# Kernel optimization log

Hardware: AMD Instinct MI355X
Metric: run time of the kernel (lower is better)

## Reference

```python
import jax, jax.numpy as jnp
import numpy as np

B, H, W = 64, 128, 128
K_SIS, K_RANGE = 0.5, 0.3
PSI_SCALE = 0.05
SKIP_W = 0.1
ALPHA_MAX = 0.5
SIGMA, KSIZE = 1.0, 5
DN = ('NCHW', 'OIHW', 'NCHW')


def conv2d(x, w, b, pad):
    y = jax.lax.conv_general_dilated(x, w, (1, 1), [(pad, pad), (pad, pad)], dimension_numbers=DN)
    return y + b[None, :, None, None]


def group_norm(x, groups, gamma, beta, eps=1e-5):
    Bc, C, Hc, Wc = x.shape
    xr = x.reshape(Bc, groups, C // groups, Hc, Wc)
    mu = xr.mean(axis=(2, 3, 4), keepdims=True)
    var = xr.var(axis=(2, 3, 4), keepdims=True)
    xn = ((xr - mu) / jnp.sqrt(var + eps)).reshape(Bc, C, Hc, Wc)
    return xn * gamma[None, :, None, None] + beta[None, :, None, None]


def coords():
    xs = jnp.linspace(-1.0, 1.0, W)
    ys = jnp.linspace(-1.0, 1.0, H)
    X, Y = jnp.meshgrid(xs, ys, indexing='xy')  # (H, W)
    r = jnp.sqrt(X * X + Y * Y)
    phi = jnp.arctan2(Y, X)
    polar = jnp.stack([r, jnp.cos(phi), jnp.sin(phi)], axis=0)  # (3,H,W)
    base_grid = jnp.stack([X, Y], axis=-1)  # (H,W,2)
    return polar, r, base_grid


def gaussian_blur(x):
    off = jnp.arange(KSIZE, dtype=jnp.float32) - (KSIZE - 1) / 2.0
    k1 = jnp.exp(-off * off / (2.0 * SIGMA * SIGMA))
    k1 = k1 / k1.sum()
    p = KSIZE // 2
    xp = jnp.pad(x, ((0, 0), (0, 0), (p, p), (p, p)), mode='reflect')
    xh = jax.lax.conv_general_dilated(xp, k1.reshape(1, 1, 1, KSIZE), (1, 1), [(0, 0), (0, 0)], dimension_numbers=DN)
    return jax.lax.conv_general_dilated(xh, k1.reshape(1, 1, KSIZE, 1), (1, 1), [(0, 0), (0, 0)], dimension_numbers=DN)


def grad_x(a, dx):  # along W (last axis), np.gradient style
    left = a[..., 1:2] - a[..., 0:1]
    mid = (a[..., 2:] - a[..., :-2]) * 0.5
    right = a[..., -1:] - a[..., -2:-1]
    return jnp.concatenate([left, mid, right], axis=-1) / dx


def grad_y(a, dy):  # along H
    top = a[..., 1:2, :] - a[..., 0:1, :]
    mid = (a[..., 2:, :] - a[..., :-2, :]) * 0.5
    bot = a[..., -1:, :] - a[..., -2:-1, :]
    return jnp.concatenate([top, mid, bot], axis=-2) / dy


def soft_clamp(a):
    return ALPHA_MAX * jnp.tanh(a / ALPHA_MAX)


def grid_sample_bilinear_border(img, grid):
    # img (B,1,H,W), grid (B,H,W,2) in [-1,1], align_corners=True, border pad
    Bc, _, Hc, Wc = img.shape
    px = (grid[..., 0] + 1.0) * 0.5 * (Wc - 1)
    py = (grid[..., 1] + 1.0) * 0.5 * (Hc - 1)
    x0 = jnp.floor(px)
    y0 = jnp.floor(py)
    wx = px - x0
    wy = py - y0
    x0i = jnp.clip(x0.astype(jnp.int32), 0, Wc - 1)
    x1i = jnp.clip(x0i + 1, 0, Wc - 1)
    y0i = jnp.clip(y0.astype(jnp.int32), 0, Hc - 1)
    y1i = jnp.clip(y0i + 1, 0, Hc - 1)
    im = img[:, 0]
    bidx = jnp.arange(Bc)[:, None, None]
    g = lambda yy, xx: im[bidx, yy, xx]
    out = (g(y0i, x0i) * (1 - wx) * (1 - wy) + g(y0i, x1i) * wx * (1 - wy)
           + g(y1i, x0i) * (1 - wx) * wy + g(y1i, x1i) * wx * wy)
    return out[:, None, :, :]


def _conv_init(key, shape, scale=None):
    fan_in = shape[1] * shape[2] * shape[3]
    s = scale if scale is not None else 1.0 / np.sqrt(fan_in)
    return jax.random.normal(key, shape, dtype=jnp.float32) * s


def setup_inputs() -> dict:
    key = jax.random.key(0)
    ks = jax.random.split(key, 16)
    d = {'image': jax.random.uniform(ks[0], (B, 1, H, W), dtype=jnp.float32)}
    # KPredictor params
    d['kw1'] = _conv_init(ks[1], (32, 4, 3, 3)); d['kb1'] = jnp.zeros((32,), jnp.float32)
    d['kg1'] = jnp.ones((32,), jnp.float32); d['kbeta1'] = jnp.zeros((32,), jnp.float32)
    d['kw2'] = _conv_init(ks[2], (32, 32, 3, 3)); d['kb2'] = jnp.zeros((32,), jnp.float32)
    d['kg2'] = jnp.ones((32,), jnp.float32); d['kbeta2'] = jnp.zeros((32,), jnp.float32)
    d['kw3'] = _conv_init(ks[3], (16, 32, 3, 3)); d['kb3'] = jnp.zeros((16,), jnp.float32)
    d['kg3'] = jnp.ones((16,), jnp.float32); d['kbeta3'] = jnp.zeros((16,), jnp.float32)
    d['kw4'] = _conv_init(ks[4], (1, 16, 1, 1), scale=0.02); d['kb4'] = jnp.zeros((1,), jnp.float32)
    # PsiResidualPredictor params
    d['pw1'] = _conv_init(ks[5], (16, 4, 3, 3)); d['pb1'] = jnp.zeros((16,), jnp.float32)
    d['pg1'] = jnp.ones((16,), jnp.float32); d['pbeta1'] = jnp.zeros((16,), jnp.float32)
    d['pw2'] = _conv_init(ks[6], (16, 16, 3, 3)); d['pb2'] = jnp.zeros((16,), jnp.float32)
    d['pg2'] = jnp.ones((16,), jnp.float32); d['pbeta2'] = jnp.zeros((16,), jnp.float32)
    d['pw3'] = _conv_init(ks[7], (1, 16, 1, 1), scale=0.02); d['pb3'] = jnp.zeros((1,), jnp.float32)
    return d


def _forward(image, kw1, kb1, kg1, kbeta1, kw2, kb2, kg2, kbeta2, kw3, kb3, kg3, kbeta3,
             kw4, kb4, pw1, pb1, pg1, pbeta1, pw2, pb2, pg2, pbeta2, pw3, pb3):
    polar, theta_abs, base_grid = coords()
    x = jnp.concatenate([image, jnp.broadcast_to(polar[None], (image.shape[0], 3, H, W))], axis=1)
    silu = jax.nn.silu
    # k predictor
    h = silu(group_norm(conv2d(x, kw1, kb1, 1), 8, kg1, kbeta1))
    h = silu(group_norm(conv2d(h, kw2, kb2, 1), 8, kg2, kbeta2))
    h = silu(group_norm(conv2d(h, kw3, kb3, 1), 4, kg3, kbeta3))
    k = K_SIS * (1.0 + K_RANGE * jnp.tanh(conv2d(h, kw4, kb4, 0)))
    # psi residual predictor
    p = silu(group_norm(conv2d(x, pw1, pb1, 1), 4, pg1, pbeta1))
    p = silu(group_norm(conv2d(p, pw2, pb2, 1), 4, pg2, pbeta2))
    psi_res = PSI_SCALE * jnp.tanh(conv2d(p, pw3, pb3, 0))
    psi = k * theta_abs[None, None] + psi_res
    psi_s = gaussian_blur(psi)
    dx = 2.0 / (W - 1)
    dy = 2.0 / (H - 1)
    alpha_x = soft_clamp(grad_x(psi_s, dx))
    alpha_y = soft_clamp(grad_y(psi_s, dy))
    alpha_grid = jnp.stack([alpha_x[:, 0], alpha_y[:, 0]], axis=-1)  # (B,H,W,2)
    beta_grid = jnp.clip(base_grid[None] - alpha_grid, -1.0, 1.0)
    warped = grid_sample_bilinear_border(image, beta_grid)
    source = (1.0 - SKIP_W) * warped + SKIP_W * image
    return source, k, psi, alpha_x, alpha_y


def reference(image, kw1, kb1, kg1, kbeta1, kw2, kb2, kg2, kbeta2, kw3, kb3, kg3, kbeta3,
              kw4, kb4, pw1, pb1, pg1, pbeta1, pw2, pb2, pg2, pbeta2, pw3, pb3):
    return _forward(image, kw1, kb1, kg1, kbeta1, kw2, kb2, kg2, kbeta2, kw3, kb3, kg3,
                    kbeta3, kw4, kb4, pw1, pb1, pg1, pbeta1, pw2, pb2, pg2, pbeta2, pw3, pb3)
```

## Files before the change

kernel.cpp:

```cpp
#include <hip/hip_runtime.h>

static constexpr int H = 128, W = 128, HW = H * W;

typedef __attribute__((ext_vector_type(8))) short short8;
typedef __attribute__((ext_vector_type(4))) float f32x4;
typedef unsigned int uint;
typedef unsigned short ushort;

__device__ __forceinline__ float silu_f(float v) { return v / (1.f + __expf(-v)); }
__device__ __forceinline__ ushort f2bf(float f) {
    uint u = __builtin_bit_cast(uint, f);
    return (ushort)((u + 0x7FFFu + ((u >> 16) & 1u)) >> 16);
}
__device__ __forceinline__ float bf2f(ushort s) {
    return __builtin_bit_cast(float, (uint)s << 16);
}

struct PrepArgs {
    const float *w1, *w2, *w3, *wp1, *wp2;
    float *wt1, *wtp1, *polar, *stats;
    ushort *wpk2h, *wpk2l, *wpk3h, *wpk3l, *wpkph, *wpkpl;
    int nstats;
};

__global__ void prep_k(PrepArgs a) {
    int tid = blockIdx.x * 256 + threadIdx.x;
    int stride = gridDim.x * 256;
    for (int i = tid; i < a.nstats; i += stride) a.stats[i] = 0.f;
    for (int i = tid; i < HW; i += stride) {
        int yy = i >> 7, xx = i & 127;
        float X = -1.f + 2.f * xx / 127.f;
        float Y = -1.f + 2.f * yy / 127.f;
        float r = sqrtf(X * X + Y * Y);
        float inv = (r > 0.f) ? 1.f / r : 0.f;
        a.polar[i] = r;
        a.polar[HW + i] = (r > 0.f) ? X * inv : 1.f;
        a.polar[2 * HW + i] = Y * inv;
    }
    for (int i = tid; i < 4 * 9 * 32; i += stride) {
        int cout = i / 36, rem = i % 36;
        a.wt1[rem * 32 + cout] = a.w1[i];
    }
    for (int i = tid; i < 4 * 9 * 16; i += stride) {
        int cout = i / 36, rem = i % 36;
        a.wtp1[rem * 16 + cout] = a.wp1[i];
    }
    for (int i = tid; i < 9 * 2 * 64 * 8; i += stride) {
        int j = i & 7, l = (i >> 3) & 63, t = i >> 9;
        int q = t >> 1, nt = t & 1;
        int k = (l >> 4) * 8 + j;
        int n = nt * 16 + (l & 15);
        int ky = q / 3, kx = q % 3;
        float w = a.w2[((n * 32 + k) * 3 + ky) * 3 + kx];
        ushort h = f2bf(w);
        a.wpk2h[i] = h;
        a.wpk2l[i] = f2bf(w - bf2f(h));
    }
    for (int i = tid; i < 9 * 64 * 8; i += stride) {
        int j = i & 7, l = (i >> 3) & 63, q = i >> 9;
        int k = (l >> 4) * 8 + j;
        int n = l & 15;
        int ky = q / 3, kx = q % 3;
        float w = a.w3[((n * 32 + k) * 3 + ky) * 3 + kx];
        ushort h = f2bf(w);
        a.wpk3h[i] = h;
        a.wpk3l[i] = f2bf(w - bf2f(h));
    }
    for (int i = tid; i < 9 * 64 * 8; i += stride) {
        int j = i & 7, l = (i >> 3) & 63, q = i >> 9;
        int k = (l >> 4) * 8 + j;
        int cin = k & 15;
        int n = l & 15;
        float w = a.wp2[((n * 16 + cin) * 3 + q / 3) * 3 + q % 3];
        ushort h = f2bf(w);
        a.wpkph[i] = h;
        a.wpkpl[i] = f2bf(w - bf2f(h));
    }
}

template <int COUT, int G>
__global__ __launch_bounds__(256) void conv1_k(
    const float* __restrict__ img, const float* __restrict__ polar,
    const float* __restrict__ wt, const float* __restrict__ bias,
    float* __restrict__ outraw, float* __restrict__ stats) {
    const int tid = threadIdx.x;
    const int y = blockIdx.x * 2 + (tid >> 7);
    const int x = tid & 127;
    const int b = blockIdx.y;

    float acc[COUT];
#pragma unroll
    for (int c = 0; c < COUT; c++) acc[c] = bias[c];

#pragma unroll
    for (int cin = 0; cin < 4; cin++) {
        const float* pl = (cin == 0) ? img + (size_t)b * HW : polar + (size_t)(cin - 1) * HW;
#pragma unroll
        for (int ky = 0; ky < 3; ky++) {
            int yy = y + ky - 1;
            if (yy >= 0 && yy < H) {
                const float* row = pl + yy * W;
                float v1 = row[x];
                float v0 = (x > 0) ? row[x - 1] : 0.f;
                float v2 = (x < 127) ? row[x + 1] : 0.f;
                const float* wr = wt + (cin * 9 + ky * 3) * COUT;
#pragma unroll
                for (int c = 0; c < COUT; c++) {
                    acc[c] = fmaf(wr[c], v0, acc[c]);
                    acc[c] = fmaf(wr[COUT + c], v1, acc[c]);
                    acc[c] = fmaf(wr[2 * COUT + c], v2, acc[c]);
                }
            }
        }
    }

    float4* ob = (float4*)(outraw + ((size_t)b * HW + y * W + x) * COUT);
#pragma unroll
    for (int i = 0; i < COUT / 4; i++)
        ob[i] = make_float4(acc[4 * i], acc[4 * i + 1], acc[4 * i + 2], acc[4 * i + 3]);

    constexpr int CgO = COUT / G;
    __shared__ float sred[4][G][2];
    const int lane = tid & 63, wid = tid >> 6;
#pragma unroll
    for (int g = 0; g < G; g++) {
        float s = 0.f, s2 = 0.f;
#pragma unroll
        for (int c = g * CgO; c < (g + 1) * CgO; c++) { s += acc[c]; s2 += acc[c] * acc[c]; }
#pragma unroll
        for (int off = 32; off > 0; off >>= 1) {
            s += __shfl_down(s, off);
            s2 += __shfl_down(s2, off);
        }
        if (lane == 0) { sred[wid][g][0] = s; sred[wid][g][1] = s2; }
    }
    __syncthreads();
    if (tid < G) {
        float s = 0.f, s2 = 0.f;
#pragma unroll
        for (int w = 0; w < 4; w++) { s += sred[w][tid][0]; s2 += sred[w][tid][1]; }
        atomicAdd(&stats[((size_t)b * G + tid) * 2], s);
        atomicAdd(&stats[((size_t)b * G + tid) * 2 + 1], s2);
    }
}

template <int CIN, int COUT, int Gin, int Gout>
__global__ __launch_bounds__(256, 3) void conv_roll_k(
    const float* __restrict__ raw_in, const float* __restrict__ stats_in,
    const float* __restrict__ gamma, const float* __restrict__ beta,
    const float* __restrict__ bias,
    const short8* __restrict__ wph, const short8* __restrict__ wpl,
    float* __restrict__ outraw, float* __restrict__ stats_out) {

    constexpr int LDSC = 2 * CIN;
    constexpr int SWZM = LDSC / 8 - 1;
    constexpr int NCH8 = CIN / 8;
    constexpr int WN = (COUT == 32) ? 2 : 1;
    constexpr int F = (WN == 2) ? 4 : 2;
    constexpr int ROWS = 8;
    constexpr int ROWB = 128 * LDSC * 2;
    constexpr int CHUNKS = 128 * NCH8 / 256;

    __shared__ __align__(16) ushort ring[3 * 128 * LDSC];
    __shared__ float la[CIN], lc[CIN];

    const int tid = threadIdx.x;
    const int wid = tid >> 6, l = tid & 63;
    const int lm = l & 15, lk = l >> 4;
    const int y0 = blockIdx.x * ROWS;
    const int b = blockIdx.y;
    const int wn = (WN == 2) ? (wid & 1) : 0;
    const int pxb = (WN == 2) ? ((wid >> 1) * 64) : (wid * 32);
    const int ch = wn * 16 + lm;

    if (tid < CIN) {
        constexpr float inv = 1.f / ((CIN / Gin) * (float)HW);
        int g = tid / (CIN / Gin);
        float s = stats_in[((size_t)b * Gin + g) * 2];
        float s2 = stats_in[((size_t)b * Gin + g) * 2 + 1];
        float m = s * inv;
        float rs = rsqrtf(s2 * inv - m * m + 1e-5f);
        float aa = gamma[tid] * rs;
        la[tid] = aa;
        lc[tid] = beta[tid] - m * aa;
    }
    __syncthreads();

    short8 wh[9], wl[9];
#pragma unroll
    for (int q = 0; q < 9; q++) {
        wh[q] = wph[(q * WN + wn) * 64 + l];
        wl[q] = wpl[(q * WN + wn) * 64 + l];
    }
    const float bv = bias[ch];
    const short8 Z8 = {0, 0, 0, 0, 0, 0, 0, 0};
    char* tbw = (char*)ring;

    auto load_row = [&](int ys, float4* g0, float4* g1) {
#pragma unroll
        for (int ck = 0; ck < CHUNKS; ck++) {
            int c = tid + ck * 256;
            int px = c / NCH8, ch8 = c % NCH8;
            const float4* gp = (const float4*)(raw_in + (((size_t)b * HW + ys * W + px) * CIN + ch8 * 8));
            g0[ck] = gp[0];
            g1[ck] = gp[1];
        }
    };
    auto stage_row = [&](int ys, int slot, const float4* g0, const float4* g1) {
#pragma unroll
        for (int ck = 0; ck < CHUNKS; ck++) {
            int c = tid + ck * 256;
            int px = c / NCH8, ch8 = c % NCH8;
            short8 hi8, lo8;
            if (ys >= 0 && ys < H) {
                float vv[8] = {g0[ck].x, g0[ck].y, g0[ck].z, g0[ck].w,
                               g1[ck].x, g1[ck].y, g1[ck].z, g1[ck].w};
#pragma unroll
                for (int e = 0; e < 8; e++) {
                    int cc = ch8 * 8 + e;
                    float f = silu_f(fmaf(vv[e], la[cc], lc[cc]));
                    ushort hb = f2bf(f);
                    hi8[e] = (short)hb;
                    lo8[e] = (short)f2bf(f - bf2f(hb));
                }
            } else {
#pragma unroll
                for (int e = 0; e < 8; e++) { hi8[e] = 0; lo8[e] = 0; }
            }
            int inner = px * LDSC * 2 + ch8 * 16;
            int swz = (px & SWZM) << 4;
            char* sb = tbw + slot * ROWB;
            *(short8*)(sb + (inner ^ swz)) = hi8;
            *(short8*)(sb + ((inner + CIN * 2) ^ swz)) = lo8;
        }
    };

    {
        float4 p0[CHUNKS], p1[CHUNKS];
        for (int pr = 0; pr < 3; pr++) {
            int ys = y0 - 1 + pr;
            if (ys >= 0 && ys < H) load_row(ys, p0, p1);
            stage_row(ys, (ys + 3) % 3, p0, p1);
        }
    }
    __syncthreads();

    float sa = 0.f, sa2 = 0.f;
    float4 g0[CHUNKS], g1[CHUNKS];

    for (int r = 0; r < ROWS; r++) {
        const int y = y0 + r;
        const int ys = y + 2;
        const bool do_stage = (r < ROWS - 1);
        if (do_stage && ys < H) load_row(ys, g0, g1);

        f32x4 acc[F];
#pragma unroll
        for (int f = 0; f < F; f++) acc[f] = (f32x4){0.f, 0.f, 0.f, 0.f};

        const char* sbase[3] = {tbw + ((y + 2) % 3) * ROWB,
                                tbw + ((y + 3) % 3) * ROWB,
                                tbw + ((y + 4) % 3) * ROWB};
#pragma unroll
        for (int q = 0; q < 9; q++) {
            const int ky = q / 3, kx = q % 3;
            const char* sb = sbase[ky];
#pragma unroll
            for (int f = 0; f < F; f++) {
                int xb = pxb + f * 16 + lm + kx - 1;
                bool valid = (xb >= 0) && (xb < 128);
                int xbc = min(max(xb, 0), 127);
                int inner = xbc * LDSC * 2;
                int swz = (xbc & SWZM) << 4;
                if constexpr (CIN == 32) {
                    short8 ah = *(const short8*)(sb + ((inner + lk * 16) ^ swz));
                    short8 al = *(const short8*)(sb + ((inner + (lk + 4) * 16) ^ swz));
                    if (!valid) { ah = Z8; al = Z8; }
                    acc[f] = __builtin_amdgcn_mfma_f32_16x16x32_bf16(ah, wh[q], acc[f], 0, 0, 0);
                    acc[f] = __builtin_amdgcn_mfma_f32_16x16x32_bf16(al, wh[q], acc[f], 0, 0, 0);
                    acc[f] = __builtin_amdgcn_mfma_f32_16x16x32_bf16(ah, wl[q], acc[f], 0, 0, 0);
                } else {
                    short8 a = *(const short8*)(sb + ((inner + lk * 16) ^ swz));
                    if (!valid) a = Z8;
                    acc[f] = __builtin_amdgcn_mfma_f32_16x16x32_bf16(a, wh[q], acc[f], 0, 0, 0);
                    acc[f] = __builtin_amdgcn_mfma_f32_16x16x32_bf16(a, wl[q], acc[f], 0, 0, 0);
                }
            }
        }

#pragma unroll
        for (int f = 0; f < F; f++) {
#pragma unroll
            for (int rr = 0; rr < 4; rr++) {
                int x = pxb + f * 16 + lk * 4 + rr;
                float v = acc[f][rr] + bv;
                outraw[((size_t)b * HW + y * W + x) * COUT + ch] = v;
                sa += v;
                sa2 += v * v;
            }
        }
        __syncthreads();
        if (do_stage) stage_row(ys, (ys + 3) % 3, g0, g1);
        __syncthreads();
    }

    float s = sa, s2 = sa2;
    s += __shfl_xor(s, 16); s2 += __shfl_xor(s2, 16);
    s += __shfl_xor(s, 32); s2 += __shfl_xor(s2, 32);
    constexpr int CgO = COUT / Gout;
#pragma unroll
    for (int m = 1; m < CgO; m <<= 1) { s += __shfl_xor(s, m); s2 += __shfl_xor(s2, m); }
    if (l < 16 && (lm & (CgO - 1)) == 0) {
        int g = ch / CgO;
        atomicAdd(&stats_out[((size_t)b * Gout + g) * 2], s);
        atomicAdd(&stats_out[((size_t)b * Gout + g) * 2 + 1], s2);
    }
}

static __device__ __constant__ float GW0 = 0.40261994689423467f;
static __device__ __constant__ float GW1 = 0.24420134200323348f;
static __device__ __constant__ float GW2 = 0.05448868454964433f;

__global__ __launch_bounds__(512) void tail_k(
    const float* __restrict__ h3, const float* __restrict__ p2,
    const float* __restrict__ img,
    const float* __restrict__ kg3, const float* __restrict__ kbeta3,
    const float* __restrict__ st3,
    const float* __restrict__ pg2, const float* __restrict__ pbeta2,
    const float* __restrict__ stp2,
    const float* __restrict__ kw4, const float* __restrict__ kb4,
    const float* __restrict__ pw3, const float* __restrict__ pb3,
    float* __restrict__ osrc, float* __restrict__ outk,
    float* __restrict__ outpsi, float* __restrict__ oax,
    float* __restrict__ oay) {
    __shared__ float psiA[38 * 128];
    __shared__ float psiB[38 * 128];

    const int tid = threadIdx.x;
    const int y0 = blockIdx.x * 32;
    const int b = blockIdx.y;

    constexpr float inv = 1.f / (float)(4 * HW);
    float a3[4], c3[4], ap[4], cp[4];
#pragma unroll
    for (int g = 0; g < 4; g++) {
        float s = st3[((size_t)b * 4 + g) * 2];
        float s2 = st3[((size_t)b * 4 + g) * 2 + 1];
        float m = s * inv;
        a3[g] = rsqrtf(s2 * inv - m * m + 1e-5f);
        c3[g] = m;
        s = stp2[((size_t)b * 4 + g) * 2];
        s2 = stp2[((size_t)b * 4 + g) * 2 + 1];
        m = s * inv;
        ap[g] = rsqrtf(s2 * inv - m * m + 1e-5f);
        cp[g] = m;
    }

    for (int idx = tid; idx < 38 * 128; idx += 512) {
        int s = idx >> 7, j = idx & 127;
        int g = y0 - 3 + s;
        g = (g < 0) ? -g : (g > 127 ? 254 - g : g);
        int rem = g * W + j;

        float hv[16], pv[16];
        const float4* hp = (const float4*)(h3 + ((size_t)b * HW + rem) * 16);
        const float4* pp = (const float4*)(p2 + ((size_t)b * HW + rem) * 16);
#pragma unroll
        for (int t = 0; t < 4; t++) {
            float4 u = hp[t];
            hv[4 * t] = u.x; hv[4 * t + 1] = u.y; hv[4 * t + 2] = u.z; hv[4 * t + 3] = u.w;
            float4 w = pp[t];
            pv[4 * t] = w.x; pv[4 * t + 1] = w.y; pv[4 * t + 2] = w.z; pv[4 * t + 3] = w.w;
        }
        float dk = kb4[0], dp = pb3[0];
#pragma unroll
        for (int c = 0; c < 16; c++) {
            int gg = c >> 2;
            float a = kg3[c] * a3[gg];
            float t = fmaf(hv[c] - c3[gg], a, kbeta3[c]);
            dk = fmaf(kw4[c], silu_f(t), dk);
            a = pg2[c] * ap[gg];
            t = fmaf(pv[c] - cp[gg], a, pbeta2[c]);
            dp = fmaf(pw3[c], silu_f(t), dp);
        }
        float k = 0.5f * (1.f + 0.3f * tanhf(dk));
        float psr = 0.05f * tanhf(dp);
        float X = -1.f + 2.f * j / 127.f;
        float Y = -1.f + 2.f * g / 127.f;
        float r = sqrtf(X * X + Y * Y);
        float psi = fmaf(k, r, psr);
        psiA[idx] = psi;
        if (s >= 3 && s <= 34) {
            int n = (size_t)b * HW + rem;
            outk[n] = k;
            outpsi[n] = psi;
        }
    }
    __syncthreads();

    for (int idx = tid; idx < 38 * 128; idx += 512) {
        int s = idx >> 7, j = idx & 127;
        const float* row = psiA + s * 128;
        int jm2 = j - 2; jm2 = jm2 < 0 ? -jm2 : jm2;
        int jm1 = j - 1; jm1 = jm1 < 0 ? -jm1 : jm1;
        int jp1 = j + 1; jp1 = jp1 > 127 ? 254 - jp1 : jp1;
        int jp2 = j + 2; jp2 = jp2 > 127 ? 254 - jp2 : jp2;
        psiB[idx] = GW2 * (row[jm2] + row[jp2]) + GW1 * (row[jm1] + row[jp1]) + GW0 * row[j];
    }
    __syncthreads();

    for (int idx = tid; idx < 34 * 128; idx += 512) {
        int s = (idx >> 7) + 2, j = idx & 127;
        psiA[s * 128 + j] = GW2 * (psiB[(s - 2) * 128 + j] + psiB[(s + 2) * 128 + j]) +
                            GW1 * (psiB[(s - 1) * 128 + j] + psiB[(s + 1) * 128 + j]) +
                            GW0 * psiB[s * 128 + j];
    }
    __syncthreads();

    const float* im = img + (size_t)b * HW;
    for (int idx = tid; idx < 32 * 128; idx += 512) {
        int r = idx >> 7, j = idx & 127;
        int y = y0 + r, s = r + 3;
        const float* ps = psiA + s * 128;

        float gx;
        if (j == 0)        gx = ps[1] - ps[0];
        else if (j == 127) gx = ps[127] - ps[126];
        else               gx = (ps[j + 1] - ps[j - 1]) * 0.5f;
        gx *= 63.5f;

        float gy;
        if (y == 0)        gy = psiA[(s + 1) * 128 + j] - ps[j];
        else if (y == 127) gy = ps[j] - psiA[(s - 1) * 128 + j];
        else               gy = (psiA[(s + 1) * 128 + j] - psiA[(s - 1) * 128 + j]) * 0.5f;
        gy *= 63.5f;

        float ax = 0.5f * tanhf(gx * 2.f);
        float ay = 0.5f * tanhf(gy * 2.f);

        float X = -1.f + 2.f * j / 127.f;
        float Y = -1.f + 2.f * y / 127.f;
        float bx = fminf(fmaxf(X - ax, -1.f), 1.f);
        float by = fminf(fmaxf(Y - ay, -1.f), 1.f);
        float px = (bx + 1.f) * 0.5f * 127.f;
        float py = (by + 1.f) * 0.5f * 127.f;
        float x0f = floorf(px), y0f = floorf(py);
        float wx = px - x0f, wy = py - y0f;
        int x0i = min(max((int)x0f, 0), 127);
        int x1i = min(x0i + 1, 127);
        int y0i = min(max((int)y0f, 0), 127);
        int y1i = min(y0i + 1, 127);

        float v00 = im[y0i * W + x0i], v01 = im[y0i * W + x1i];
        float v10 = im[y1i * W + x0i], v11 = im[y1i * W + x1i];
        float wrp = v00 * (1.f - wx) * (1.f - wy) + v01 * wx * (1.f - wy) +
                    v10 * (1.f - wx) * wy + v11 * wx * wy;

        int n = (size_t)b * HW + y * W + j;
        osrc[n] = 0.9f * wrp + 0.1f * im[y * W + j];
        oax[n] = ax;
        oay[n] = ay;
    }
}

extern "C" void kernel_launch(void* const* d_in, const int* in_sizes, int n_in,
                              void* d_out, int out_size, void* d_ws, size_t ws_size,
                              hipStream_t stream) {
    const float* img = (const float*)d_in[0];
    const int B = in_sizes[0] / HW;
    const int npix = B * HW;

    char* base = (char*)d_ws;
    size_t off = 0;
    auto alloc = [&](size_t bytes) {
        char* p = base + off;
        off = (off + bytes + 255) & ~(size_t)255;
        return p;
    };

    float* polar = (float*)alloc(3 * HW * 4);
    float* wt1   = (float*)alloc(4 * 9 * 32 * 4);
    float* wtp1  = (float*)alloc(4 * 9 * 16 * 4);
    ushort* wpk2h = (ushort*)alloc(9 * 2 * 64 * 8 * 2);
    ushort* wpk2l = (ushort*)alloc(9 * 2 * 64 * 8 * 2);
    ushort* wpk3h = (ushort*)alloc(9 * 64 * 8 * 2);
    ushort* wpk3l = (ushort*)alloc(9 * 64 * 8 * 2);
    ushort* wpkph = (ushort*)alloc(9 * 64 * 8 * 2);
    ushort* wpkpl = (ushort*)alloc(9 * 64 * 8 * 2);
    int nstats = B * 56;
    float* stats = (float*)alloc((size_t)nstats * 4);
    float* st1  = stats;
    float* st2  = st1 + (size_t)B * 16;
    float* st3  = st2 + (size_t)B * 16;
    float* stp1 = st3 + (size_t)B * 8;
    float* stp2 = stp1 + (size_t)B * 8;
    size_t head = off;

    int BC = B;
    while (BC > 1) {
        size_t need = head + 2 * ((size_t)BC * HW * 32 * 4 + 256);
        if (need <= ws_size) break;
        BC >>= 1;
    }
    float* R  = (float*)alloc((size_t)BC * HW * 32 * 4);
    float* R2 = (float*)alloc((size_t)BC * HW * 32 * 4);
    float* h3R = R;
    float* p2R = R + (size_t)BC * HW * 16;
    float* RpR = R2;

    float* outsrc = (float*)d_out;
    float* outk   = outsrc + (size_t)npix;
    float* outpsi = outk + (size_t)npix;
    float* outax  = outpsi + (size_t)npix;
    float* outay  = outax + (size_t)npix;

    PrepArgs pa;
    pa.w1 = (const float*)d_in[1]; pa.w2 = (const float*)d_in[5];
    pa.w3 = (const float*)d_in[9]; pa.wp1 = (const float*)d_in[15];
    pa.wp2 = (const float*)d_in[19];
    pa.wt1 = wt1; pa.wtp1 = wtp1; pa.polar = polar; pa.stats = stats;
    pa.wpk2h = wpk2h; pa.wpk2l = wpk2l; pa.wpk3h = wpk3h; pa.wpk3l = wpk3l;
    pa.wpkph = wpkph; pa.wpkpl = wpkpl; pa.nstats = nstats;
    prep_k<<<128, 256, 0, stream>>>(pa);

    for (int b0 = 0; b0 < B; b0 += BC) {
        const float* imgc = img + (size_t)b0 * HW;
        dim3 cg1(H / 2, BC), cgr(H / 8, BC);

        conv1_k<32, 8><<<cg1, 256, 0, stream>>>(imgc, polar, wt1, (const float*)d_in[2],
                                                R, st1 + (size_t)b0 * 16);
        conv_roll_k<32, 32, 8, 8><<<cgr, 256, 0, stream>>>(
            R, st1 + (size_t)b0 * 16, (const float*)d_in[3], (const float*)d_in[4],
            (const float*)d_in[6], (const short8*)wpk2h, (const short8*)wpk2l,
            R2, st2 + (size_t)b0 * 16);
        conv_roll_k<32, 16, 8, 4><<<cgr, 256, 0, stream>>>(
            R2, st2 + (size_t)b0 * 16, (const float*)d_in[7], (const float*)d_in[8],
            (const float*)d_in[10], (const short8*)wpk3h, (const short8*)wpk3l,
            h3R, st3 + (size_t)b0 * 8);

        conv1_k<16, 4><<<cg1, 256, 0, stream>>>(imgc, polar, wtp1, (const float*)d_in[16],
                                                RpR, stp1 + (size_t)b0 * 8);
        conv_roll_k<16, 16, 4, 4><<<cgr, 256, 0, stream>>>(
            RpR, stp1 + (size_t)b0 * 8, (const float*)d_in[17], (const float*)d_in[18],
            (const float*)d_in[20], (const short8*)wpkph, (const short8*)wpkpl,
            p2R, stp2 + (size_t)b0 * 8);

        tail_k<<<dim3(4, BC), 512, 0, stream>>>(
            h3R, p2R, imgc,
            (const float*)d_in[11], (const float*)d_in[12], st3 + (size_t)b0 * 8,
            (const float*)d_in[21], (const float*)d_in[22], stp2 + (size_t)b0 * 8,
            (const float*)d_in[13], (const float*)d_in[14],
            (const float*)d_in[23], (const float*)d_in[24],
            outsrc + (size_t)b0 * HW, outk + (size_t)b0 * HW,
            outpsi + (size_t)b0 * HW, outax + (size_t)b0 * HW,
            outay + (size_t)b0 * HW);
    }
}
```

Baseline: 462.1 us.

## Fuse both first-layer convs into one kernel, shrink tail tiles, fast tanh

Merges the two first-layer convolutions (32 and 16 output channels) into a single kernel that reads the image and polar inputs once and writes both outputs and group stats. To make room, the buffer layout gets a separate p2 buffer and the psi branch is reordered to run before the k branch. The tail kernel now uses 16-row tiles instead of 32, doubling the number of blocks at the cost of more halo recomputation. tanh and silu now use an exp plus hardware reciprocal formulation, which may lose a little accuracy. The 48-channel accumulator raises register pressure in the fused conv.

```diff
diff --git a/kernel.cpp b/kernel.cpp
--- a/kernel.cpp
+++ b/kernel.cpp
@@ -7,7 +7,9 @@
 typedef unsigned int uint;
 typedef unsigned short ushort;
 
-__device__ __forceinline__ float silu_f(float v) { return v / (1.f + __expf(-v)); }
+__device__ __forceinline__ float rcp_f(float x) { return __builtin_amdgcn_rcpf(x); }
+__device__ __forceinline__ float silu_f(float v) { return v * rcp_f(1.f + __expf(-v)); }
+__device__ __forceinline__ float tanh_f(float x) { return 1.f - 2.f * rcp_f(__expf(2.f * x) + 1.f); }
 __device__ __forceinline__ ushort f2bf(float f) {
     uint u = __builtin_bit_cast(uint, f);
     return (ushort)((u + 0x7FFFu + ((u >> 16) & 1u)) >> 16);
@@ -18,7 +20,7 @@
 
 struct PrepArgs {
     const float *w1, *w2, *w3, *wp1, *wp2;
-    float *wt1, *wtp1, *polar, *stats;
+    float *wt48, *polar, *stats;
     ushort *wpk2h, *wpk2l, *wpk3h, *wpk3l, *wpkph, *wpkpl;
     int nstats;
 };
@@ -37,13 +39,12 @@
         a.polar[HW + i] = (r > 0.f) ? X * inv : 1.f;
         a.polar[2 * HW + i] = Y * inv;
     }
-    for (int i = tid; i < 4 * 9 * 32; i += stride) {
-        int cout = i / 36, rem = i % 36;
-        a.wt1[rem * 32 + cout] = a.w1[i];
-    }
-    for (int i = tid; i < 4 * 9 * 16; i += stride) {
-        int cout = i / 36, rem = i % 36;
-        a.wtp1[rem * 16 + cout] = a.wp1[i];
+    for (int i = tid; i < 36 * 48; i += stride) {
+        int t = i / 48, c = i % 48;
+        int cin = t / 9, k = t % 9;
+        float w = (c < 32) ? a.w1[((c * 4 + cin) * 3 + k / 3) * 3 + k % 3]
+                           : a.wp1[(((c - 32) * 4 + cin) * 3 + k / 3) * 3 + k % 3];
+        a.wt48[i] = w;
     }
     for (int i = tid; i < 9 * 2 * 64 * 8; i += stride) {
         int j = i & 7, l = (i >> 3) & 63, t = i >> 9;
@@ -78,19 +79,22 @@
     }
 }
 
-template <int COUT, int G>
-__global__ __launch_bounds__(256) void conv1_k(
+__global__ __launch_bounds__(256) void conv1f_k(
     const float* __restrict__ img, const float* __restrict__ polar,
-    const float* __restrict__ wt, const float* __restrict__ bias,
-    float* __restrict__ outraw, float* __restrict__ stats) {
+    const float* __restrict__ wt48,
+    const float* __restrict__ kb1, const float* __restrict__ pb1,
+    float* __restrict__ outK, float* __restrict__ outP,
+    float* __restrict__ st1, float* __restrict__ stp1) {
     const int tid = threadIdx.x;
     const int y = blockIdx.x * 2 + (tid >> 7);
     const int x = tid & 127;
     const int b = blockIdx.y;
 
-    float acc[COUT];
-#pragma unroll
-    for (int c = 0; c < COUT; c++) acc[c] = bias[c];
+    float acc[48];
+#pragma unroll
+    for (int c = 0; c < 32; c++) acc[c] = kb1[c];
+#pragma unroll
+    for (int c = 0; c < 16; c++) acc[32 + c] = pb1[c];
 
 #pragma unroll
     for (int cin = 0; cin < 4; cin++) {
@@ -103,30 +107,33 @@
                 float v1 = row[x];
                 float v0 = (x > 0) ? row[x - 1] : 0.f;
                 float v2 = (x < 127) ? row[x + 1] : 0.f;
-                const float* wr = wt + (cin * 9 + ky * 3) * COUT;
-#pragma unroll
-                for (int c = 0; c < COUT; c++) {
+                const float* wr = wt48 + (cin * 9 + ky * 3) * 48;
+#pragma unroll
+                for (int c = 0; c < 48; c++) {
                     acc[c] = fmaf(wr[c], v0, acc[c]);
-                    acc[c] = fmaf(wr[COUT + c], v1, acc[c]);
-                    acc[c] = fmaf(wr[2 * COUT + c], v2, acc[c]);
+                    acc[c] = fmaf(wr[48 + c], v1, acc[c]);
+                    acc[c] = fmaf(wr[96 + c], v2, acc[c]);
                 }
             }
         }
     }
 
-    float4* ob = (float4*)(outraw + ((size_t)b * HW + y * W + x) * COUT);
-#pragma unroll
-    for (int i = 0; i < COUT / 4; i++)
-        ob[i] = make_float4(acc[4 * i], acc[4 * i + 1], acc[4 * i + 2], acc[4 * i + 3]);
-
-    constexpr int CgO = COUT / G;
-    __shared__ float sred[4][G][2];
+    float4* obK = (float4*)(outK + ((size_t)b * HW + y * W + x) * 32);
+#pragma unroll
+    for (int i = 0; i < 8; i++)
+        obK[i] = make_float4(acc[4 * i], acc[4 * i + 1], acc[4 * i + 2], acc[4 * i + 3]);
+    float4* obP = (float4*)(outP + ((size_t)b * HW + y * W + x) * 16);
+#pragma unroll
+    for (int i = 0; i < 4; i++)
+        obP[i] = make_float4(acc[32 + 4 * i], acc[33 + 4 * i], acc[34 + 4 * i], acc[35 + 4 * i]);
+
+    __shared__ float sred[4][12][2];
     const int lane = tid & 63, wid = tid >> 6;
 #pragma unroll
-    for (int g = 0; g < G; g++) {
+    for (int g = 0; g < 12; g++) {
         float s = 0.f, s2 = 0.f;
 #pragma unroll
-        for (int c = g * CgO; c < (g + 1) * CgO; c++) { s += acc[c]; s2 += acc[c] * acc[c]; }
+        for (int c = g * 4; c < g * 4 + 4; c++) { s += acc[c]; s2 += acc[c] * acc[c]; }
 #pragma unroll
         for (int off = 32; off > 0; off >>= 1) {
             s += __shfl_down(s, off);
@@ -135,12 +142,14 @@
         if (lane == 0) { sred[wid][g][0] = s; sred[wid][g][1] = s2; }
     }
     __syncthreads();
-    if (tid < G) {
+    if (tid < 12) {
         float s = 0.f, s2 = 0.f;
 #pragma unroll
         for (int w = 0; w < 4; w++) { s += sred[w][tid][0]; s2 += sred[w][tid][1]; }
-        atomicAdd(&stats[((size_t)b * G + tid) * 2], s);
-        atomicAdd(&stats[((size_t)b * G + tid) * 2 + 1], s2);
+        float* dst = (tid < 8) ? &st1[((size_t)b * 8 + tid) * 2]
+                               : &stp1[((size_t)b * 4 + (tid - 8)) * 2];
+        atomicAdd(dst, s);
+        atomicAdd(dst + 1, s2);
     }
 }
 
@@ -333,11 +342,11 @@
     float* __restrict__ osrc, float* __restrict__ outk,
     float* __restrict__ outpsi, float* __restrict__ oax,
     float* __restrict__ oay) {
-    __shared__ float psiA[38 * 128];
-    __shared__ float psiB[38 * 128];
+    __shared__ float psiA[22 * 128];
+    __shared__ float psiB[22 * 128];
 
     const int tid = threadIdx.x;
-    const int y0 = blockIdx.x * 32;
+    const int y0 = blockIdx.x * 16;
     const int b = blockIdx.y;
 
     constexpr float inv = 1.f / (float)(4 * HW);
@@ -356,7 +365,7 @@
         cp[g] = m;
     }
 
-    for (int idx = tid; idx < 38 * 128; idx += 512) {
+    for (int idx = tid; idx < 22 * 128; idx += 512) {
         int s = idx >> 7, j = idx & 127;
         int g = y0 - 3 + s;
         g = (g < 0) ? -g : (g > 127 ? 254 - g : g);
@@ -383,14 +392,14 @@
             t = fmaf(pv[c] - cp[gg], a, pbeta2[c]);
             dp = fmaf(pw3[c], silu_f(t), dp);
         }
-        float k = 0.5f * (1.f + 0.3f * tanhf(dk));
-        float psr = 0.05f * tanhf(dp);
+        float k = 0.5f * (1.f + 0.3f * tanh_f(dk));
+        float psr = 0.05f * tanh_f(dp);
         float X = -1.f + 2.f * j / 127.f;
         float Y = -1.f + 2.f * g / 127.f;
         float r = sqrtf(X * X + Y * Y);
         float psi = fmaf(k, r, psr);
         psiA[idx] = psi;
-        if (s >= 3 && s <= 34) {
+        if (s >= 3 && s < 19) {
             int n = (size_t)b * HW + rem;
             outk[n] = k;
             outpsi[n] = psi;
@@ -398,7 +407,7 @@
     }
     __syncthreads();
 
-    for (int idx = tid; idx < 38 * 128; idx += 512) {
+    for (int idx = tid; idx < 22 * 128; idx += 512) {
         int s = idx >> 7, j = idx & 127;
         const float* row = psiA + s * 128;
         int jm2 = j - 2; jm2 = jm2 < 0 ? -jm2 : jm2;
@@ -409,7 +418,7 @@
     }
     __syncthreads();
 
-    for (int idx = tid; idx < 34 * 128; idx += 512) {
+    for (int idx = tid; idx < 18 * 128; idx += 512) {
         int s = (idx >> 7) + 2, j = idx & 127;
         psiA[s * 128 + j] = GW2 * (psiB[(s - 2) * 128 + j] + psiB[(s + 2) * 128 + j]) +
                             GW1 * (psiB[(s - 1) * 128 + j] + psiB[(s + 1) * 128 + j]) +
@@ -418,7 +427,7 @@
     __syncthreads();
 
     const float* im = img + (size_t)b * HW;
-    for (int idx = tid; idx < 32 * 128; idx += 512) {
+    for (int idx = tid; idx < 16 * 128; idx += 512) {
         int r = idx >> 7, j = idx & 127;
         int y = y0 + r, s = r + 3;
         const float* ps = psiA + s * 128;
@@ -435,8 +444,8 @@
         else               gy = (psiA[(s + 1) * 128 + j] - psiA[(s - 1) * 128 + j]) * 0.5f;
         gy *= 63.5f;
 
-        float ax = 0.5f * tanhf(gx * 2.f);
-        float ay = 0.5f * tanhf(gy * 2.f);
+        float ax = 0.5f * tanh_f(gx * 2.f);
+        float ay = 0.5f * tanh_f(gy * 2.f);
 
         float X = -1.f + 2.f * j / 127.f;
         float Y = -1.f + 2.f * y / 127.f;
@@ -479,8 +488,7 @@
     };
 
     float* polar = (float*)alloc(3 * HW * 4);
-    float* wt1   = (float*)alloc(4 * 9 * 32 * 4);
-    float* wtp1  = (float*)alloc(4 * 9 * 16 * 4);
+    float* wt48  = (float*)alloc(36 * 48 * 4);
     ushort* wpk2h = (ushort*)alloc(9 * 2 * 64 * 8 * 2);
     ushort* wpk2l = (ushort*)alloc(9 * 2 * 64 * 8 * 2);
     ushort* wpk3h = (ushort*)alloc(9 * 64 * 8 * 2);
@@ -498,15 +506,15 @@
 
     int BC = B;
     while (BC > 1) {
-        size_t need = head + 2 * ((size_t)BC * HW * 32 * 4 + 256);
+        size_t need = head + (size_t)BC * HW * 80 * 4 + 3 * 256;
         if (need <= ws_size) break;
         BC >>= 1;
     }
-    float* R  = (float*)alloc((size_t)BC * HW * 32 * 4);
-    float* R2 = (float*)alloc((size_t)BC * HW * 32 * 4);
-    float* h3R = R;
-    float* p2R = R + (size_t)BC * HW * 16;
-    float* RpR = R2;
+    float* R   = (float*)alloc((size_t)BC * HW * 32 * 4);
+    float* R2  = (float*)alloc((size_t)BC * HW * 32 * 4);
+    float* p2B = (float*)alloc((size_t)BC * HW * 16 * 4);
+    float* RpB = R2;
+    float* h3B = R;
 
     float* outsrc = (float*)d_out;
     float* outk   = outsrc + (size_t)npix;
@@ -518,17 +526,24 @@
     pa.w1 = (const float*)d_in[1]; pa.w2 = (const float*)d_in[5];
     pa.w3 = (const float*)d_in[9]; pa.wp1 = (const float*)d_in[15];
     pa.wp2 = (const float*)d_in[19];
-    pa.wt1 = wt1; pa.wtp1 = wtp1; pa.polar = polar; pa.stats = stats;
+    pa.wt48 = wt48; pa.polar = polar; pa.stats = stats;
     pa.wpk2h = wpk2h; pa.wpk2l = wpk2l; pa.wpk3h = wpk3h; pa.wpk3l = wpk3l;
     pa.wpkph = wpkph; pa.wpkpl = wpkpl; pa.nstats = nstats;
     prep_k<<<128, 256, 0, stream>>>(pa);
 
     for (int b0 = 0; b0 < B; b0 += BC) {
         const float* imgc = img + (size_t)b0 * HW;
-        dim3 cg1(H / 2, BC), cgr(H / 8, BC);
-
-        conv1_k<32, 8><<<cg1, 256, 0, stream>>>(imgc, polar, wt1, (const float*)d_in[2],
-                                                R, st1 + (size_t)b0 * 16);
+        dim3 cgf(H / 2, BC), cgr(H / 8, BC);
+
+        conv1f_k<<<cgf, 256, 0, stream>>>(imgc, polar, wt48,
+                                          (const float*)d_in[2], (const float*)d_in[16],
+                                          R, RpB, st1 + (size_t)b0 * 16, stp1 + (size_t)b0 * 8);
+
+        conv_roll_k<16, 16, 4, 4><<<cgr, 256, 0, stream>>>(
+            RpB, stp1 + (size_t)b0 * 8, (const float*)d_in[17], (const float*)d_in[18],
+            (const float*)d_in[20], (const short8*)wpkph, (const short8*)wpkpl,
+            p2B, stp2 + (size_t)b0 * 8);
+
         conv_roll_k<32, 32, 8, 8><<<cgr, 256, 0, stream>>>(
             R, st1 + (size_t)b0 * 16, (const float*)d_in[3], (const float*)d_in[4],
             (const float*)d_in[6], (const short8*)wpk2h, (const short8*)wpk2l,
@@ -536,17 +551,10 @@
         conv_roll_k<32, 16, 8, 4><<<cgr, 256, 0, stream>>>(
             R2, st2 + (size_t)b0 * 16, (const float*)d_in[7], (const float*)d_in[8],
             (const float*)d_in[10], (const short8*)wpk3h, (const short8*)wpk3l,
-            h3R, st3 + (size_t)b0 * 8);
-
-        conv1_k<16, 4><<<cg1, 256, 0, stream>>>(imgc, polar, wtp1, (const float*)d_in[16],
-                                                RpR, stp1 + (size_t)b0 * 8);
-        conv_roll_k<16, 16, 4, 4><<<cgr, 256, 0, stream>>>(
-            RpR, stp1 + (size_t)b0 * 8, (const float*)d_in[17], (const float*)d_in[18],
-            (const float*)d_in[20], (const short8*)wpkph, (const short8*)wpkpl,
-            p2R, stp2 + (size_t)b0 * 8);
-
-        tail_k<<<dim3(4, BC), 512, 0, stream>>>(
-            h3R, p2R, imgc,
+            h3B, st3 + (size_t)b0 * 8);
+
+        tail_k<<<dim3(8, BC), 512, 0, stream>>>(
+            h3B, p2B, imgc,
             (const float*)d_in[11], (const float*)d_in[12], st3 + (size_t)b0 * 8,
             (const float*)d_in[21], (const float*)d_in[22], stp2 + (size_t)b0 * 8,
             (const float*)d_in[13], (const float*)d_in[14],
```

Measured after the change: 379.0 us (median of 2 runs). -18.0%, faster.
